# Performance work log

Hardware: AMD Instinct MI355X
Metric: run time of the kernel (lower is better)

Reference implementation:

```python
import jax, jax.numpy as jnp
import numpy as np

ATTN_HEADS = 4
NEG_INF = float(np.finfo(np.float32).min)


def setup_inputs() -> dict:
    key = jax.random.key(0)
    ks = jax.random.split(key, 7)
    B, N, K, Cin, Cout = 4, 4096, 32, 128, 128
    h_X = jax.random.normal(ks[0], (B, N, Cout), dtype=jnp.float32)
    h_E = jax.random.normal(ks[1], (B, N, K, Cin), dtype=jnp.float32)
    mask_attn = jax.random.randint(ks[2], (B, N, K), 0, 2, dtype=jnp.int32)
    # torch Linear weights are [out_features, in_features]
    W_Q = jax.random.normal(ks[3], (Cout, Cout), dtype=jnp.float32) / np.sqrt(Cout)
    W_K = jax.random.normal(ks[4], (Cout, Cin), dtype=jnp.float32) / np.sqrt(Cin)
    W_V = jax.random.normal(ks[5], (Cout, Cin), dtype=jnp.float32) / np.sqrt(Cin)
    W_O = jax.random.normal(ks[6], (Cout, 3 * Cout), dtype=jnp.float32) / np.sqrt(3 * Cout)
    return {"h_X": h_X, "h_E": h_E, "mask_attn": mask_attn,
            "W_Q": W_Q, "W_K": W_K, "W_V": W_V, "W_O": W_O}


def reference(h_X, h_E, mask_attn, W_Q, W_K, W_V, W_O):
    B, N, K, _ = h_E.shape
    C = W_Q.shape[0]
    H = ATTN_HEADS
    d = C // H

    h_q = (h_X @ W_Q.T).reshape(B, N, H, d)          # [B,N,H,d]
    h_k = (h_E @ W_K.T).reshape(B, N, K, H, d)       # [B,N,K,H,d]
    h_v = (h_E @ W_V.T).reshape(B, N, K, H, d)       # [B,N,K,H,d]

    # per-node, per-head scores over K neighbors
    scores = jnp.einsum('bnhd,bnkhd->bnhk', h_q, h_k) / np.sqrt(d)

    mask = (mask_attn[:, :, None, :] > 0)            # [B,N,1,K] -> broadcast over heads
    logits = jnp.where(mask, scores, NEG_INF)
    attn = jax.nn.softmax(logits, axis=-1) * mask.astype(scores.dtype)  # [B,N,H,K]

    attn_sum = attn.sum(axis=-1, keepdims=True) + 1e-8                  # [B,N,H,1]
    hv_t = jnp.swapaxes(h_v, 2, 3)                                      # [B,N,H,K,d]
    weighted_v = attn[..., None] * hv_t                                 # [B,N,H,K,d]
    weighted_sum = weighted_v.sum(axis=3)                               # [B,N,H,d]
    aggr_mean = (weighted_sum / attn_sum).reshape(B, N, C)
    aggr_sum = weighted_sum.reshape(B, N, C)
    aggr_max = weighted_v.max(axis=3).reshape(B, N, C)

    aggr_cat = jnp.concatenate([aggr_mean, aggr_sum, aggr_max], axis=-1)  # [B,N,3C]
    return aggr_cat @ W_O.T                                               # [B,N,C]
```

## Files before the change

kernel.cpp:

```cpp
#include <hip/hip_runtime.h>
#include <hip/hip_bf16.h>
#include <stdint.h>


typedef __attribute__((ext_vector_type(8))) short short8;
typedef __attribute__((ext_vector_type(4))) float f32x4;

#define NPB   16
#define CDIM  128
#define KN    32
#define ESTR  136
#define CATS  392
#define NEGI  -3.0e38f

__device__ __forceinline__ float bf2f(short s) {
    union { unsigned int u; float f; } v;
    v.u = ((unsigned int)(unsigned short)s) << 16;
    return v.f;
}
__device__ __forceinline__ short f2bf(float f) {
    union { float ff; unsigned int u; } v; v.ff = f;
    unsigned int u = v.u;
    u += 0x7FFFu + ((u >> 16) & 1u);
    return (short)(u >> 16);
}

__device__ __forceinline__ short8 cvt8(const f32x4& a, const f32x4& b) {
    union { __hip_bfloat162 h; unsigned int u; } c0, c1, c2, c3;
    c0.h = __float22bfloat162_rn(float2{a[0], a[1]});
    c1.h = __float22bfloat162_rn(float2{a[2], a[3]});
    c2.h = __float22bfloat162_rn(float2{b[0], b[1]});
    c3.h = __float22bfloat162_rn(float2{b[2], b[3]});
    short8 r;
    r[0] = (short)(c0.u & 0xffff); r[1] = (short)(c0.u >> 16);
    r[2] = (short)(c1.u & 0xffff); r[3] = (short)(c1.u >> 16);
    r[4] = (short)(c2.u & 0xffff); r[5] = (short)(c2.u >> 16);
    r[6] = (short)(c3.u & 0xffff); r[7] = (short)(c3.u >> 16);
    return r;
}

template<bool FP32>
__device__ __forceinline__ short8 load8bf(const void* p, size_t idx) {
    if constexpr (FP32) {
        const float* fp = (const float*)p + idx;
        f32x4 a = *(const f32x4*)fp;
        f32x4 b = *(const f32x4*)(fp + 4);
        return cvt8(a, b);
    } else {
        return *(const short8*)((const short*)p + idx);
    }
}

template<bool FP32>
__device__ __forceinline__ short loadbf1(const void* p, size_t idx) {
    if constexpr (FP32) return f2bf(((const float*)p)[idx]);
    else return ((const short*)p)[idx];
}

__device__ __forceinline__ bool detect_fp32(const short* wp) {
    const int lane = threadIdx.x & 63;
    int cnt = 0;
    #pragma unroll
    for (int i = 0; i < 8; ++i) {
        const float v = bf2f(wp[lane + i * 64]);
        if (!(fabsf(v) < 8.0f)) cnt++;
    }
    #pragma unroll
    for (int d = 1; d < 64; d <<= 1) cnt += __shfl_xor(cnt, d);
    return cnt > 16;
}

struct alignas(16) Smem {
    short sEb[2][32 * ESTR];
    short sT[64 * ESTR];
    union {
        short sQ[16 * ESTR];
        short sCat[16 * CATS];
    } u;
    int      sMask[NPB * KN];
    unsigned sMaskBits[NPB];
};

template<bool FP32>
__device__ __forceinline__ void issueN(const void* hE, size_t base, int tid,
                                       f32x4 (&pF)[2][2], short8 (&pB)[2]) {
    if constexpr (FP32) {
        #pragma unroll
        for (int it = 0; it < 2; ++it) {
            const float* p = (const float*)hE + base + (size_t)(it * 256 + tid) * 8;
            pF[it][0] = *(const f32x4*)p;
            pF[it][1] = *(const f32x4*)(p + 4);
        }
    } else {
        #pragma unroll
        for (int it = 0; it < 2; ++it)
            pB[it] = *(const short8*)((const short*)hE + base + (size_t)(it * 256 + tid) * 8);
    }
    __builtin_amdgcn_sched_barrier(0);
}

template<bool FP32>
__device__ __forceinline__ void writeN(short* dst, int tid,
                                       const f32x4 (&pF)[2][2], const short8 (&pB)[2]) {
    #pragma unroll
    for (int it = 0; it < 2; ++it) {
        const int chunk = it * 256 + tid, row = chunk >> 4, cc = chunk & 15;
        short8 v;
        if constexpr (FP32) v = cvt8(pF[it][0], pF[it][1]);
        else                v = pB[it];
        *(short8*)&dst[row * ESTR + cc * 8] = v;
    }
}

template<bool FP32>
__device__ __forceinline__ void na_body(Smem& sm,
    const void* __restrict__ hX, const void* __restrict__ hE,
    const int* __restrict__ mask, const void* __restrict__ WQ,
    const void* __restrict__ WK, const void* __restrict__ WV,
    const void* __restrict__ WO, void* __restrict__ out)
{
    const int tid  = threadIdx.x;
    const int lane = tid & 63;
    const int w    = tid >> 6;
    const int quad = lane >> 4;
    const int l15  = lane & 15;
    const int nb   = blockIdx.x * NPB;
    const size_t ebase = (size_t)nb * (KN * CDIM);

    f32x4 pF[2][2]; short8 pB[2];
    issueN<FP32>(hE, ebase, tid, pF, pB);

    *(int2*)&sm.sMask[tid * 2] = *(const int2*)&mask[(size_t)nb * KN + tid * 2];

    short8 ax[4];
    #pragma unroll
    for (int kk = 0; kk < 4; ++kk)
        ax[kk] = load8bf<FP32>(hX, (size_t)(nb + l15) * CDIM + kk * 32 + quad * 8);
    short8 bq[2][4];
    #pragma unroll
    for (int t2 = 0; t2 < 2; ++t2)
        #pragma unroll
        for (int kk = 0; kk < 4; ++kk)
            bq[t2][kk] = load8bf<FP32>(WQ, (size_t)(w * 32 + t2 * 16 + l15) * CDIM + kk * 32 + quad * 8);
    {
        f32x4 o0 = {0.f,0.f,0.f,0.f}, o1 = {0.f,0.f,0.f,0.f};
        #pragma unroll
        for (int kk = 0; kk < 4; ++kk) {
            o0 = __builtin_amdgcn_mfma_f32_16x16x32_bf16(ax[kk], bq[0][kk], o0, 0, 0, 0);
            o1 = __builtin_amdgcn_mfma_f32_16x16x32_bf16(ax[kk], bq[1][kk], o1, 0, 0, 0);
        }
        #pragma unroll
        for (int r = 0; r < 4; ++r) {
            const int n = quad * 4 + r;
            sm.u.sQ[n * ESTR + w * 32 + l15]      = f2bf(o0[r]);
            sm.u.sQ[n * ESTR + w * 32 + 16 + l15] = f2bf(o1[r]);
        }
    }
    __syncthreads();

    #pragma unroll
    for (int t = 0; t < 4; ++t) {
        const int n = w * 4 + t;
        const bool bit = (lane < 32) && (sm.sMask[n * KN + (lane & 31)] > 0);
        const unsigned long long bal = __ballot(bit);
        if (lane == 0) sm.sMaskBits[n] = (unsigned)bal;
    }

    short8 bk[2][4];
    #pragma unroll
    for (int t2 = 0; t2 < 2; ++t2)
        #pragma unroll
        for (int kk = 0; kk < 4; ++kk) {
            const int j = w * 32 + t2 * 16 + l15;
            short8 b;
            #pragma unroll
            for (int jj = 0; jj < 8; ++jj)
                b[jj] = loadbf1<FP32>(WK, (size_t)(kk * 32 + quad * 8 + jj) * CDIM + j);
            bk[t2][kk] = b;
        }
    {
        const float scale = 0.17677669529663687f;
        const short8 zz = {0,0,0,0,0,0,0,0};
        #pragma unroll
        for (int m = 0; m < 4; ++m) {
            const int n_g = m * 4 + (l15 >> 2), h_ = l15 & 3;
            const short8 qv = *(const short8*)&sm.u.sQ[n_g * ESTR + h_ * 32 + quad * 8];
            f32x4 c0 = {0.f,0.f,0.f,0.f}, c1 = {0.f,0.f,0.f,0.f};
            #pragma unroll
            for (int kk = 0; kk < 4; ++kk) {
                const short8 af = (kk == h_) ? qv : zz;
                c0 = __builtin_amdgcn_mfma_f32_16x16x32_bf16(af, bk[0][kk], c0, 0, 0, 0);
                c1 = __builtin_amdgcn_mfma_f32_16x16x32_bf16(af, bk[1][kk], c1, 0, 0, 0);
            }
            #pragma unroll
            for (int r = 0; r < 4; ++r) {
                const int row = m * 16 + quad * 4 + r;
                sm.sT[row * ESTR + w * 32 + l15]      = f2bf(c0[r] * scale);
                sm.sT[row * ESTR + w * 32 + 16 + l15] = f2bf(c1[r] * scale);
            }
        }
    }

    short8 bv[2][4];
    #pragma unroll
    for (int ct2 = 0; ct2 < 2; ++ct2)
        #pragma unroll
        for (int kk = 0; kk < 4; ++kk)
            bv[ct2][kk] = load8bf<FP32>(WV, (size_t)((2 * w + ct2) * 16 + l15) * CDIM + kk * 32 + quad * 8);

    writeN<FP32>(sm.sEb[0], tid, pF, pB);
    issueN<FP32>(hE, ebase + 1 * (KN * CDIM), tid, pF, pB);
    __syncthreads();

    #pragma unroll 1
    for (int i = 0; i < NPB; ++i) {
        const short* bufp = sm.sEb[i & 1];

        short8 a0[4], a1[4], bs[4];
        #pragma unroll
        for (int kk = 0; kk < 4; ++kk) {
            bs[kk] = *(const short8*)&sm.sT[(i * 4 + w) * ESTR + kk * 32 + quad * 8];
            a0[kk] = *(const short8*)&bufp[l15 * ESTR + kk * 32 + quad * 8];
            a1[kk] = *(const short8*)&bufp[(16 + l15) * ESTR + kk * 32 + quad * 8];
        }

        f32x4 s0 = {0.f,0.f,0.f,0.f}, s1 = {0.f,0.f,0.f,0.f};
        #pragma unroll
        for (int kk = 0; kk < 4; ++kk) {
            s0 = __builtin_amdgcn_mfma_f32_16x16x32_bf16(a0[kk], bs[kk], s0, 0, 0, 0);
            s1 = __builtin_amdgcn_mfma_f32_16x16x32_bf16(a1[kk], bs[kk], s1, 0, 0, 0);
        }

        float x[8], ainv;
        {
            const unsigned mb = sm.sMaskBits[i];
            float m = NEGI;
            #pragma unroll
            for (int j = 0; j < 4; ++j) {
                x[j]     = s0[j];
                x[4 + j] = s1[j];
                m = fmaxf(m, ((mb >> (quad * 4 + j)) & 1u)      ? s0[j] : NEGI);
                m = fmaxf(m, ((mb >> (16 + quad * 4 + j)) & 1u) ? s1[j] : NEGI);
            }
            m = fmaxf(m, __shfl_xor(m, 16));
            m = fmaxf(m, __shfl_xor(m, 32));
            float dsum = 0.f;
            #pragma unroll
            for (int j = 0; j < 4; ++j) {
                const float e0 = __expf(fminf(x[j] - m, 0.f))
                                 * (((mb >> (quad * 4 + j)) & 1u) ? 1.f : 0.f);
                const float e1 = __expf(fminf(x[4 + j] - m, 0.f))
                                 * (((mb >> (16 + quad * 4 + j)) & 1u) ? 1.f : 0.f);
                x[j] = e0; x[4 + j] = e1;
                dsum += e0 + e1;
            }
            dsum += __shfl_xor(dsum, 16);
            dsum += __shfl_xor(dsum, 32);
            const float inv = (dsum > 0.f) ? (1.f / dsum) : 0.f;
            #pragma unroll
            for (int j = 0; j < 8; ++j) x[j] *= inv;
            ainv = 1.0f / (((dsum > 0.f) ? 1.0f : 0.0f) + 1e-8f);
        }

        if (i < NPB - 1) {
            writeN<FP32>(sm.sEb[(i + 1) & 1], tid, pF, pB);
            if (i < NPB - 2)
                issueN<FP32>(hE, ebase + (size_t)(i + 2) * (KN * CDIM), tid, pF, pB);
        }

        #pragma unroll
        for (int ct2 = 0; ct2 < 2; ++ct2) {
            f32x4 av0 = {0.f,0.f,0.f,0.f}, av1 = {0.f,0.f,0.f,0.f};
            #pragma unroll
            for (int kk = 0; kk < 4; ++kk) {
                av0 = __builtin_amdgcn_mfma_f32_16x16x32_bf16(a0[kk], bv[ct2][kk], av0, 0, 0, 0);
                av1 = __builtin_amdgcn_mfma_f32_16x16x32_bf16(a1[kk], bv[ct2][kk], av1, 0, 0, 0);
            }
            float sum = 0.f, mx = NEGI;
            #pragma unroll
            for (int r = 0; r < 4; ++r) {
                const float p0 = x[r]     * av0[r];
                const float p1 = x[4 + r] * av1[r];
                sum += p0 + p1;
                mx = fmaxf(mx, fmaxf(p0, p1));
            }
            sum += __shfl_xor(sum, 16);
            sum += __shfl_xor(sum, 32);
            mx = fmaxf(mx, __shfl_xor(mx, 16));
            mx = fmaxf(mx, __shfl_xor(mx, 32));
            if (quad == 0) {
                const int c = (2 * w + ct2) * 16 + l15;
                sm.u.sCat[i * CATS + c]       = f2bf(sum * ainv);
                sm.u.sCat[i * CATS + 128 + c] = f2bf(sum);
                sm.u.sCat[i * CATS + 256 + c] = f2bf(mx);
            }
        }

        asm volatile("s_waitcnt lgkmcnt(0)" ::: "memory");
        __builtin_amdgcn_s_barrier();
        __builtin_amdgcn_sched_barrier(0);
    }
    __syncthreads();

    {
        f32x4 o0 = {0.f,0.f,0.f,0.f}, o1 = {0.f,0.f,0.f,0.f};
        #pragma unroll
        for (int kk = 0; kk < 12; ++kk) {
            const short8 a  = *(const short8*)&sm.u.sCat[l15 * CATS + kk * 32 + quad * 8];
            const short8 b0 = load8bf<FP32>(WO, (size_t)(w * 32 + l15) * 384 + kk * 32 + quad * 8);
            const short8 b1 = load8bf<FP32>(WO, (size_t)(w * 32 + 16 + l15) * 384 + kk * 32 + quad * 8);
            o0 = __builtin_amdgcn_mfma_f32_16x16x32_bf16(a, b0, o0, 0, 0, 0);
            o1 = __builtin_amdgcn_mfma_f32_16x16x32_bf16(a, b1, o1, 0, 0, 0);
        }
        #pragma unroll
        for (int r = 0; r < 4; ++r) {
            const int node = quad * 4 + r;
            const size_t base = (size_t)(nb + node) * CDIM + w * 32;
            if constexpr (FP32) {
                ((float*)out)[base + l15]      = o0[r];
                ((float*)out)[base + 16 + l15] = o1[r];
            } else {
                ((short*)out)[base + l15]      = f2bf(o0[r]);
                ((short*)out)[base + 16 + l15] = f2bf(o1[r]);
            }
        }
    }
}

__global__ __launch_bounds__(256, 2)
void na_fused(const void* __restrict__ hX, const void* __restrict__ hE,
              const int* __restrict__ mask, const void* __restrict__ WQ,
              const void* __restrict__ WK, const void* __restrict__ WV,
              const void* __restrict__ WO, void* __restrict__ out)
{
    __shared__ Smem sm;
    if (detect_fp32((const short*)WQ)) na_body<true >(sm, hX, hE, mask, WQ, WK, WV, WO, out);
    else                               na_body<false>(sm, hX, hE, mask, WQ, WK, WV, WO, out);
}

extern "C" void kernel_launch(void* const* d_in, const int* in_sizes, int n_in,
                              void* d_out, int out_size, void* d_ws, size_t ws_size,
                              hipStream_t stream) {
    (void)in_sizes; (void)n_in; (void)ws_size; (void)out_size; (void)d_ws;
    const void* hX   = d_in[0];
    const void* hE   = d_in[1];
    const int*  mask = (const int*)d_in[2];
    const void* WQ   = d_in[3];
    const void* WK   = d_in[4];
    const void* WV   = d_in[5];
    const void* WO   = d_in[6];

    na_fused<<<dim3(1024), dim3(256), 0, stream>>>(hX, hE, mask, WQ, WK, WV, WO, d_out);
}
```

Before: 397.2 us.

## Process neighbor edge tiles in pairs per pipeline stage to halve barriers

```diff
diff --git a/kernel.cpp b/kernel.cpp
--- a/kernel.cpp
+++ b/kernel.cpp
@@ -71,7 +71,7 @@
 }
 
 struct alignas(16) Smem {
-    short sEb[2][32 * ESTR];
+    short sEb[2][64 * ESTR];
     short sT[64 * ESTR];
     union {
         short sQ[16 * ESTR];
@@ -82,28 +82,28 @@
 };
 
 template<bool FP32>
-__device__ __forceinline__ void issueN(const void* hE, size_t base, int tid,
-                                       f32x4 (&pF)[2][2], short8 (&pB)[2]) {
+__device__ __forceinline__ void issueP(const void* hE, size_t base, int tid,
+                                       f32x4 (&pF)[4][2], short8 (&pB)[4]) {
     if constexpr (FP32) {
         #pragma unroll
-        for (int it = 0; it < 2; ++it) {
+        for (int it = 0; it < 4; ++it) {
             const float* p = (const float*)hE + base + (size_t)(it * 256 + tid) * 8;
             pF[it][0] = *(const f32x4*)p;
             pF[it][1] = *(const f32x4*)(p + 4);
         }
     } else {
         #pragma unroll
-        for (int it = 0; it < 2; ++it)
+        for (int it = 0; it < 4; ++it)
             pB[it] = *(const short8*)((const short*)hE + base + (size_t)(it * 256 + tid) * 8);
     }
     __builtin_amdgcn_sched_barrier(0);
 }
 
 template<bool FP32>
-__device__ __forceinline__ void writeN(short* dst, int tid,
-                                       const f32x4 (&pF)[2][2], const short8 (&pB)[2]) {
-    #pragma unroll
-    for (int it = 0; it < 2; ++it) {
+__device__ __forceinline__ void writeP(short* dst, int tid,
+                                       const f32x4 (&pF)[4][2], const short8 (&pB)[4]) {
+    #pragma unroll
+    for (int it = 0; it < 4; ++it) {
         const int chunk = it * 256 + tid, row = chunk >> 4, cc = chunk & 15;
         short8 v;
         if constexpr (FP32) v = cvt8(pF[it][0], pF[it][1]);
@@ -127,8 +127,8 @@
     const int nb   = blockIdx.x * NPB;
     const size_t ebase = (size_t)nb * (KN * CDIM);
 
-    f32x4 pF[2][2]; short8 pB[2];
-    issueN<FP32>(hE, ebase, tid, pF, pB);
+    f32x4 pF[4][2]; short8 pB[4];
+    issueP<FP32>(hE, ebase, tid, pF, pB);
 
     *(int2*)&sm.sMask[tid * 2] = *(const int2*)&mask[(size_t)nb * KN + tid * 2];
 
@@ -208,91 +208,99 @@
         for (int kk = 0; kk < 4; ++kk)
             bv[ct2][kk] = load8bf<FP32>(WV, (size_t)((2 * w + ct2) * 16 + l15) * CDIM + kk * 32 + quad * 8);
 
-    writeN<FP32>(sm.sEb[0], tid, pF, pB);
-    issueN<FP32>(hE, ebase + 1 * (KN * CDIM), tid, pF, pB);
+    writeP<FP32>(sm.sEb[0], tid, pF, pB);
+    issueP<FP32>(hE, ebase + 2 * (KN * CDIM), tid, pF, pB);
     __syncthreads();
 
     #pragma unroll 1
-    for (int i = 0; i < NPB; ++i) {
-        const short* bufp = sm.sEb[i & 1];
-
-        short8 a0[4], a1[4], bs[4];
-        #pragma unroll
-        for (int kk = 0; kk < 4; ++kk) {
-            bs[kk] = *(const short8*)&sm.sT[(i * 4 + w) * ESTR + kk * 32 + quad * 8];
-            a0[kk] = *(const short8*)&bufp[l15 * ESTR + kk * 32 + quad * 8];
-            a1[kk] = *(const short8*)&bufp[(16 + l15) * ESTR + kk * 32 + quad * 8];
-        }
-
-        f32x4 s0 = {0.f,0.f,0.f,0.f}, s1 = {0.f,0.f,0.f,0.f};
-        #pragma unroll
-        for (int kk = 0; kk < 4; ++kk) {
-            s0 = __builtin_amdgcn_mfma_f32_16x16x32_bf16(a0[kk], bs[kk], s0, 0, 0, 0);
-            s1 = __builtin_amdgcn_mfma_f32_16x16x32_bf16(a1[kk], bs[kk], s1, 0, 0, 0);
-        }
-
-        float x[8], ainv;
-        {
-            const unsigned mb = sm.sMaskBits[i];
-            float m = NEGI;
-            #pragma unroll
-            for (int j = 0; j < 4; ++j) {
-                x[j]     = s0[j];
-                x[4 + j] = s1[j];
-                m = fmaxf(m, ((mb >> (quad * 4 + j)) & 1u)      ? s0[j] : NEGI);
-                m = fmaxf(m, ((mb >> (16 + quad * 4 + j)) & 1u) ? s1[j] : NEGI);
-            }
-            m = fmaxf(m, __shfl_xor(m, 16));
-            m = fmaxf(m, __shfl_xor(m, 32));
-            float dsum = 0.f;
-            #pragma unroll
-            for (int j = 0; j < 4; ++j) {
-                const float e0 = __expf(fminf(x[j] - m, 0.f))
-                                 * (((mb >> (quad * 4 + j)) & 1u) ? 1.f : 0.f);
-                const float e1 = __expf(fminf(x[4 + j] - m, 0.f))
-                                 * (((mb >> (16 + quad * 4 + j)) & 1u) ? 1.f : 0.f);
-                x[j] = e0; x[4 + j] = e1;
-                dsum += e0 + e1;
-            }
-            dsum += __shfl_xor(dsum, 16);
-            dsum += __shfl_xor(dsum, 32);
-            const float inv = (dsum > 0.f) ? (1.f / dsum) : 0.f;
-            #pragma unroll
-            for (int j = 0; j < 8; ++j) x[j] *= inv;
-            ainv = 1.0f / (((dsum > 0.f) ? 1.0f : 0.0f) + 1e-8f);
-        }
-
-        if (i < NPB - 1) {
-            writeN<FP32>(sm.sEb[(i + 1) & 1], tid, pF, pB);
-            if (i < NPB - 2)
-                issueN<FP32>(hE, ebase + (size_t)(i + 2) * (KN * CDIM), tid, pF, pB);
-        }
-
-        #pragma unroll
-        for (int ct2 = 0; ct2 < 2; ++ct2) {
-            f32x4 av0 = {0.f,0.f,0.f,0.f}, av1 = {0.f,0.f,0.f,0.f};
+    for (int ip = 0; ip < NPB / 2; ++ip) {
+        const short* bufp = sm.sEb[ip & 1];
+
+        #pragma unroll
+        for (int j = 0; j < 2; ++j) {
+            const int nl = ip * 2 + j;
+            const short* nbuf = bufp + j * 32 * ESTR;
+
+            short8 a0[4], a1[4], bs[4];
             #pragma unroll
             for (int kk = 0; kk < 4; ++kk) {
-                av0 = __builtin_amdgcn_mfma_f32_16x16x32_bf16(a0[kk], bv[ct2][kk], av0, 0, 0, 0);
-                av1 = __builtin_amdgcn_mfma_f32_16x16x32_bf16(a1[kk], bv[ct2][kk], av1, 0, 0, 0);
-            }
-            float sum = 0.f, mx = NEGI;
-            #pragma unroll
-            for (int r = 0; r < 4; ++r) {
-                const float p0 = x[r]     * av0[r];
-                const float p1 = x[4 + r] * av1[r];
-                sum += p0 + p1;
-                mx = fmaxf(mx, fmaxf(p0, p1));
-            }
-            sum += __shfl_xor(sum, 16);
-            sum += __shfl_xor(sum, 32);
-            mx = fmaxf(mx, __shfl_xor(mx, 16));
-            mx = fmaxf(mx, __shfl_xor(mx, 32));
-            if (quad == 0) {
-                const int c = (2 * w + ct2) * 16 + l15;
-                sm.u.sCat[i * CATS + c]       = f2bf(sum * ainv);
-                sm.u.sCat[i * CATS + 128 + c] = f2bf(sum);
-                sm.u.sCat[i * CATS + 256 + c] = f2bf(mx);
+                bs[kk] = *(const short8*)&sm.sT[(nl * 4 + w) * ESTR + kk * 32 + quad * 8];
+                a0[kk] = *(const short8*)&nbuf[l15 * ESTR + kk * 32 + quad * 8];
+                a1[kk] = *(const short8*)&nbuf[(16 + l15) * ESTR + kk * 32 + quad * 8];
+            }
+
+            f32x4 s0 = {0.f,0.f,0.f,0.f}, s1 = {0.f,0.f,0.f,0.f};
+            #pragma unroll
+            for (int kk = 0; kk < 4; ++kk) {
+                s0 = __builtin_amdgcn_mfma_f32_16x16x32_bf16(a0[kk], bs[kk], s0, 0, 0, 0);
+                s1 = __builtin_amdgcn_mfma_f32_16x16x32_bf16(a1[kk], bs[kk], s1, 0, 0, 0);
+            }
+
+            float x[8], ainv;
+            {
+                const unsigned mb = sm.sMaskBits[nl];
+                float m = NEGI;
+                #pragma unroll
+                for (int jj = 0; jj < 4; ++jj) {
+                    x[jj]     = s0[jj];
+                    x[4 + jj] = s1[jj];
+                    m = fmaxf(m, ((mb >> (quad * 4 + jj)) & 1u)      ? s0[jj] : NEGI);
+                    m = fmaxf(m, ((mb >> (16 + quad * 4 + jj)) & 1u) ? s1[jj] : NEGI);
+                }
+                m = fmaxf(m, __shfl_xor(m, 16));
+                m = fmaxf(m, __shfl_xor(m, 32));
+                float dsum = 0.f;
+                #pragma unroll
+                for (int jj = 0; jj < 4; ++jj) {
+                    const float e0 = __expf(fminf(x[jj] - m, 0.f))
+                                     * (((mb >> (quad * 4 + jj)) & 1u) ? 1.f : 0.f);
+                    const float e1 = __expf(fminf(x[4 + jj] - m, 0.f))
+                                     * (((mb >> (16 + quad * 4 + jj)) & 1u) ? 1.f : 0.f);
+                    x[jj] = e0; x[4 + jj] = e1;
+                    dsum += e0 + e1;
+                }
+                dsum += __shfl_xor(dsum, 16);
+                dsum += __shfl_xor(dsum, 32);
+                const float inv = (dsum > 0.f) ? (1.f / dsum) : 0.f;
+                #pragma unroll
+                for (int jj = 0; jj < 8; ++jj) x[jj] *= inv;
+                ainv = 1.0f / (((dsum > 0.f) ? 1.0f : 0.0f) + 1e-8f);
+            }
+
+            if (j == 0) {
+                if (ip < NPB / 2 - 1) {
+                    writeP<FP32>(sm.sEb[(ip + 1) & 1], tid, pF, pB);
+                    if (ip < NPB / 2 - 2)
+                        issueP<FP32>(hE, ebase + (size_t)(ip + 2) * 2 * (KN * CDIM), tid, pF, pB);
+                }
+            }
+
+            #pragma unroll
+            for (int ct2 = 0; ct2 < 2; ++ct2) {
+                f32x4 av0 = {0.f,0.f,0.f,0.f}, av1 = {0.f,0.f,0.f,0.f};
+                #pragma unroll
+                for (int kk = 0; kk < 4; ++kk) {
+                    av0 = __builtin_amdgcn_mfma_f32_16x16x32_bf16(a0[kk], bv[ct2][kk], av0, 0, 0, 0);
+                    av1 = __builtin_amdgcn_mfma_f32_16x16x32_bf16(a1[kk], bv[ct2][kk], av1, 0, 0, 0);
+                }
+                float sum = 0.f, mx = NEGI;
+                #pragma unroll
+                for (int r = 0; r < 4; ++r) {
+                    const float p0 = x[r]     * av0[r];
+                    const float p1 = x[4 + r] * av1[r];
+                    sum += p0 + p1;
+                    mx = fmaxf(mx, fmaxf(p0, p1));
+                }
+                sum += __shfl_xor(sum, 16);
+                sum += __shfl_xor(sum, 32);
+                mx = fmaxf(mx, __shfl_xor(mx, 16));
+                mx = fmaxf(mx, __shfl_xor(mx, 32));
+                if (quad == 0) {
+                    const int c = (2 * w + ct2) * 16 + l15;
+                    sm.u.sCat[nl * CATS + c]       = f2bf(sum * ainv);
+                    sm.u.sCat[nl * CATS + 128 + c] = f2bf(sum);
+                    sm.u.sCat[nl * CATS + 256 + c] = f2bf(mx);
+                }
             }
         }
 
```

Result: no change. 403.7 us (+1.6%).
